# Kernel tuning notes

Hardware: AMD Instinct MI355X
Metric: run time of the kernel (lower is better)

Reference implementation:

```python
import jax, jax.numpy as jnp
import numpy as np
from jax import lax

EPS = 1e-20
BN_EPS = 1e-5
ATTN_SCALE = 2.8284271247461903  # sqrt(d_l=8)
NS = (32, 32, 32, 10)
DS = (8, 8, 8, 16)


def squash(x):
    # Efficient-CapsNet squash: (1 - 1/(exp(||x||)+eps)) * x/(||x||+eps)
    norm = jnp.linalg.norm(x, axis=-1, keepdims=True)
    return (1.0 - 1.0 / (jnp.exp(norm) + EPS)) * (x / (norm + EPS))


def conv2d(x, w, b, stride, groups=1):
    y = lax.conv_general_dilated(
        x, w, window_strides=(stride, stride), padding='VALID',
        dimension_numbers=('NCHW', 'OIHW', 'NCHW'),
        feature_group_count=groups)
    return y + b[None, :, None, None]


def bn(x, g, b, m, v):
    inv = g / jnp.sqrt(v + BN_EPS)
    return x * inv[None, :, None, None] + (b - m * inv)[None, :, None, None]


def fccaps(U_l, W):
    # U_l: (b, n_l, d_l), W: (n_l, n_h, d_l, d_h)
    U_hat = jnp.einsum('bij,ikjl->bikl', U_l, W)          # (b, n_l, n_h, d_h)
    A = jnp.einsum('bikl,bhkl->bhik', U_hat, U_hat)        # (b, n_l, n_l, n_h)
    A_sum = jnp.sum(A, axis=-2)                            # (b, n_l, n_h)
    C = jax.nn.softmax(A_sum / ATTN_SCALE, axis=-1)        # (b, n_l, n_h)
    U_h = jnp.einsum('bikl,bik->bkl', U_hat, C)            # (b, n_h, d_h)
    return squash(U_h)


def setup_inputs() -> dict:
    key = jax.random.key(0)
    ks = jax.random.split(key, 8)
    B = 512
    x = jax.random.normal(ks[0], (B, 1, 39, 39), dtype=jnp.float32)
    conv1_w = jax.random.normal(ks[1], (128, 1, 3, 3), jnp.float32) * 0.2
    conv1_b = jnp.zeros((128,), jnp.float32)
    conv2_w = jax.random.normal(ks[2], (256, 128, 3, 3), jnp.float32) * 0.04
    conv2_b = jnp.zeros((256,), jnp.float32)
    conv3_w = jax.random.normal(ks[3], (256, 1, 9, 9), jnp.float32) * 0.1  # depthwise
    conv3_b = jnp.zeros((256,), jnp.float32)
    bn1_g = jnp.ones((128,), jnp.float32); bn1_b = jnp.zeros((128,), jnp.float32)
    bn1_m = jnp.zeros((128,), jnp.float32); bn1_v = jnp.ones((128,), jnp.float32)
    bn2_g = jnp.ones((256,), jnp.float32); bn2_b = jnp.zeros((256,), jnp.float32)
    bn2_m = jnp.zeros((256,), jnp.float32); bn2_v = jnp.ones((256,), jnp.float32)
    # capsule weights, kaiming-ish scale sqrt(2/fan_in) with fan_in = n_h*d_l*d_h
    def caps_w(k, n_l, n_h, d_l, d_h):
        std = np.sqrt(2.0 / (n_h * d_l * d_h))
        return jax.random.normal(k, (n_l, n_h, d_l, d_h), jnp.float32) * std
    W1 = caps_w(ks[4], NS[0], NS[1], DS[0], DS[1])
    W2 = caps_w(ks[5], NS[1], NS[2], DS[1], DS[2])
    W3 = caps_w(ks[6], NS[2], NS[3], DS[2], DS[3])
    return dict(x=x, conv1_w=conv1_w, conv1_b=conv1_b,
                bn1_g=bn1_g, bn1_b=bn1_b, bn1_m=bn1_m, bn1_v=bn1_v,
                conv2_w=conv2_w, conv2_b=conv2_b,
                bn2_g=bn2_g, bn2_b=bn2_b, bn2_m=bn2_m, bn2_v=bn2_v,
                conv3_w=conv3_w, conv3_b=conv3_b, W1=W1, W2=W2, W3=W3)


def reference(x, conv1_w, conv1_b, bn1_g, bn1_b, bn1_m, bn1_v,
              conv2_w, conv2_b, bn2_g, bn2_b, bn2_m, bn2_v,
              conv3_w, conv3_b, W1, W2, W3):
    h = jax.nn.relu(bn(conv2d(x, conv1_w, conv1_b, 2), bn1_g, bn1_b, bn1_m, bn1_v))
    h = jax.nn.relu(bn(conv2d(h, conv2_w, conv2_b, 2), bn2_g, bn2_b, bn2_m, bn2_v))
    h = conv2d(h, conv3_w, conv3_b, 1, groups=256)        # (B, 256, 1, 1)
    u = h.reshape(h.shape[0], NS[0], DS[0])                # (B, 32, 8)
    u = squash(u)
    for W in (W1, W2, W3):
        u = fccaps(u, W)
    return u  # (B, 10, 16)
```

## Files before the change

kernel.cpp:

```cpp
#include <hip/hip_runtime.h>


typedef __attribute__((ext_vector_type(8))) short short8;
typedef __attribute__((ext_vector_type(4))) float f32x4;

__device__ __forceinline__ ushort f2bf(float x) {
    uint u = __float_as_uint(x);
    return (ushort)((u + 0x7FFFu + ((u >> 16) & 1u)) >> 16);
}
__device__ __forceinline__ void bfsplit(float x, ushort& h, ushort& l) {
    h = f2bf(x);
    float hf = __uint_as_float(((uint)h) << 16);
    l = f2bf(x - hf);
}

__global__ __launch_bounds__(256) void k_prep(
    const float* __restrict__ w2, uint* __restrict__ Bt,
    const float* __restrict__ w3, float* __restrict__ w3T,
    const float* __restrict__ W1, const float* __restrict__ W2,
    const float* __restrict__ W3, float* __restrict__ Wr1,
    float* __restrict__ Wr2, float* __restrict__ Wr3) {
    __shared__ __align__(16) float wbuf[64 * 288];
    const int b = blockIdx.x, t = threadIdx.x;
    if (b < 144) {
        const int sidx = b >> 2, coq = b & 3;
        const int chunk = sidx / 9, tap = sidx - chunk * 9;
        const int co0 = coq * 64;
        for (int idx = t; idx < 4608; idx += 256) {
            const int n = idx / 72, q = idx - n * 72;
            ((float4*)wbuf)[n * 72 + q] =
                *(const float4*)(w2 + (size_t)(co0 + n) * 1152 + chunk * 288 + q * 4);
        }
        __syncthreads();
        const int n = t & 63, dg = (t >> 6) * 4;
        const int cot = coq >> 1, nn = ((coq & 1) * 64) + n;
        uint* dst = Bt + (size_t)(sidx * 2 + cot) * 4096;
#pragma unroll
        for (int dd = 0; dd < 4; ++dd) {
            const int d = dg + dd;
            const float x = wbuf[n * 288 + (2 * d) * 9 + tap];
            const float y = wbuf[n * 288 + (2 * d + 1) * 9 + tap];
            ushort xh, xl, yh, yl;
            bfsplit(x, xh, xl);
            bfsplit(y, yl == yl ? yh : yh, yl);
            bfsplit(y, yh, yl);
            dst[nn * 16 + d]        = (uint)xh | ((uint)yh << 16);
            dst[2048 + nn * 16 + d] = (uint)xl | ((uint)yl << 16);
        }
    } else if (b < 225) {
        const int p = b - 144;
        w3T[p * 256 + t] = w3[t * 81 + p];
    } else {
        const int bb = b - 225;
        const int layer = bb >> 5, blk = bb & 31;
        const float* src = layer == 0 ? W1 : (layer == 1 ? W2 : W3);
        float* dst = layer == 0 ? Wr1 : (layer == 1 ? Wr2 : Wr3);
        const int d_h = (layer == 2) ? 16 : 8;
        const int total = (layer == 2) ? 5120 : 8192;
        for (int idx = blk * 256 + t; idx < 8 * total; idx += 32 * 256) {
            const int j = idx / total, e = idx - j * total;
            const int ik = e / d_h, l = e - ik * d_h;
            dst[idx] = src[(ik * 8 + j) * d_h + l];
        }
    }
}

__global__ __launch_bounds__(256) void k_conv1(
    const float* __restrict__ x, const float* __restrict__ w,
    const float* __restrict__ bias, const float* __restrict__ g,
    const float* __restrict__ bb, const float* __restrict__ bm,
    const float* __restrict__ bv, ushort* __restrict__ h1) {
    __shared__ __align__(16) float xs[1521];
    __shared__ float wls[1152];
    __shared__ float2 scsh[128];
    const int b = blockIdx.x, t = threadIdx.x;
    const float* xb = x + (size_t)b * 1521;
    for (int i = t; i < 1521; i += 256) xs[i] = xb[i];
    for (int i = t; i < 1152; i += 256) wls[i] = w[i];
    if (t < 128) {
        const float inv = g[t] * rsqrtf(bv[t] + 1e-5f);
        scsh[t] = make_float2(inv, bias[t] * inv + bb[t] - bm[t] * inv);
    }
    __syncthreads();
    const int o = t & 15, pg = t >> 4;
    float wr[8][9];
#pragma unroll
    for (int j = 0; j < 8; ++j)
#pragma unroll
        for (int k = 0; k < 9; ++k) wr[j][k] = wls[(o * 8 + j) * 9 + k];
    float2 ss[8];
#pragma unroll
    for (int j = 0; j < 8; ++j) ss[j] = scsh[o * 8 + j];
    const int chunk = o >> 2, ol = o & 3;
    ushort* cb = h1 + (size_t)b * 92416 + chunk * 23104;
    for (int p = pg; p < 361; p += 16) {
        const int y = p / 19, xq = p - y * 19;
        const int base = y * 78 + xq * 2;
        const float x0 = xs[base],      x1 = xs[base + 1],  x2 = xs[base + 2];
        const float x3 = xs[base + 39], x4 = xs[base + 40], x5 = xs[base + 41];
        const float x6 = xs[base + 78], x7 = xs[base + 79], x8 = xs[base + 80];
        short8 hs, ls;
#pragma unroll
        for (int j = 0; j < 8; ++j) {
            const float acc = x0 * wr[j][0] + x1 * wr[j][1] + x2 * wr[j][2] +
                              x3 * wr[j][3] + x4 * wr[j][4] + x5 * wr[j][5] +
                              x6 * wr[j][6] + x7 * wr[j][7] + x8 * wr[j][8];
            const float v = fmaxf(fmaf(acc, ss[j].x, ss[j].y), 0.0f);
            ushort hh, lw;
            bfsplit(v, hh, lw);
            hs[j] = (short)hh;
            ls[j] = (short)lw;
        }
        if ((xq & 1) == 0) {
            const int pos = y * 10 + (xq >> 1);
            *(short8*)(cb + ol * 1520 + pos * 8)         = hs;
            *(short8*)(cb + 11552 + ol * 1520 + pos * 8) = ls;
        } else {
            const int pos = y * 9 + (xq >> 1);
            *(short8*)(cb + 6080 + ol * 1368 + pos * 8)  = hs;
            *(short8*)(cb + 17632 + ol * 1368 + pos * 8) = ls;
        }
    }
}

__global__ __launch_bounds__(256, 3) void k_conv2(
    const uint* __restrict__ h1u, const uint* __restrict__ Bt,
    const float* __restrict__ g,
    const float* __restrict__ bb, const float* __restrict__ bm,
    const float* __restrict__ bv, const float* __restrict__ bias,
    const float* __restrict__ w3T, float* __restrict__ Uws) {
    __shared__ __align__(16) uint raw[11552];
    __shared__ float ured[128];
    const int t = threadIdx.x;
    const int lane = t & 63, wave = t >> 6;
    const int ln15 = lane & 15, lq = lane >> 4;
    const int wm = (wave >> 1) * 48, wn = (wave & 1) * 64;
    const int gg = blockIdx.x;
    const int bi  = ((gg >> 4) << 3) | (gg & 7);
    const int cot = (gg >> 3) & 1;
    const int co0 = cot * 128;

    int PE[3], PO[3];
#pragma unroll
    for (int i = 0; i < 3; ++i) {
        const int m = wm + i * 16 + ln15;
        const int p = m < 81 ? m : 80;
        const int oh = p / 9, ow = p - oh * 9;
        PE[i] = lq * 760 + oh * 80 + ow * 4;
        PO[i] = 3040 + lq * 684 + oh * 72 + ow * 4;
    }
    int BRDg[4];
#pragma unroll
    for (int j = 0; j < 4; ++j) {
        const int n = wn + j * 16 + ln15;
        BRDg[j] = n * 16 + lq * 4;
    }

    f32x4 acc[3][4] = {};
    uint4 Bn[8];
    {
        const uint* bp = Bt + (size_t)cot * 4096;
#pragma unroll
        for (int j = 0; j < 4; ++j) {
            Bn[j]     = *(const uint4*)(bp + BRDg[j]);
            Bn[4 + j] = *(const uint4*)(bp + 2048 + BRDg[j]);
        }
    }

#pragma unroll
    for (int c = 0; c < 4; ++c) {
        __syncthreads();
        {
            const uint4* src = (const uint4*)(h1u + (size_t)(bi * 4 + c) * 11552);
            uint4* dst = (uint4*)raw;
            uint4 tmp[11];
#pragma unroll
            for (int k = 0; k < 11; ++k) tmp[k] = src[t + k * 256];
            const bool extra = (t < 72);
            uint4 te;
            if (extra) te = src[t + 11 * 256];
#pragma unroll
            for (int k = 0; k < 11; ++k) dst[t + k * 256] = tmp[k];
            if (extra) dst[t + 11 * 256] = te;
        }
        __syncthreads();
        short8 a_h[3];
#pragma unroll
        for (int i = 0; i < 3; ++i)
            a_h[i] = *reinterpret_cast<const short8*>(raw + PE[i]);
#pragma unroll
        for (int tap = 0; tap < 9; ++tap) {
            const int s = c * 9 + tap;
            uint4 Bc[8];
#pragma unroll
            for (int q = 0; q < 8; ++q) Bc[q] = Bn[q];
            if (s < 35) {
                const uint* bp = Bt + (size_t)((s + 1) * 2 + cot) * 4096;
#pragma unroll
                for (int j = 0; j < 4; ++j) {
                    Bn[j]     = *(const uint4*)(bp + BRDg[j]);
                    Bn[4 + j] = *(const uint4*)(bp + 2048 + BRDg[j]);
                }
            }
            const int kh = tap / 3, kw = tap - kh * 3;
            const int odd = kw & 1;
            const int sE = kh * 40 + (kw >> 1) * 4;
            const int sO = kh * 36;
            short8 a_l[3];
#pragma unroll
            for (int i = 0; i < 3; ++i) {
                const int addr = odd ? (PO[i] + sO) : (PE[i] + sE);
                a_l[i] = *reinterpret_cast<const short8*>(raw + addr + 5776);
            }
            short8 a_hn[3];
            if (tap < 8) {
                const int tap2 = tap + 1;
                const int kh2 = tap2 / 3, kw2 = tap2 - kh2 * 3;
                const int odd2 = kw2 & 1;
                const int sE2 = kh2 * 40 + (kw2 >> 1) * 4;
                const int sO2 = kh2 * 36;
#pragma unroll
                for (int i = 0; i < 3; ++i) {
                    const int addr2 = odd2 ? (PO[i] + sO2) : (PE[i] + sE2);
                    a_hn[i] = *reinterpret_cast<const short8*>(raw + addr2);
                }
            }
            short8 bh[4], bl[4];
#pragma unroll
            for (int j = 0; j < 4; ++j) {
                bh[j] = __builtin_bit_cast(short8, Bc[j]);
                bl[j] = __builtin_bit_cast(short8, Bc[4 + j]);
            }
#pragma unroll
            for (int i = 0; i < 3; ++i)
#pragma unroll
                for (int j = 0; j < 4; ++j)
                    acc[i][j] = __builtin_amdgcn_mfma_f32_16x16x32_bf16(a_h[i], bh[j], acc[i][j], 0, 0, 0);
#pragma unroll
            for (int i = 0; i < 3; ++i)
#pragma unroll
                for (int j = 0; j < 4; ++j)
                    acc[i][j] = __builtin_amdgcn_mfma_f32_16x16x32_bf16(a_h[i], bl[j], acc[i][j], 0, 0, 0);
#pragma unroll
            for (int i = 0; i < 3; ++i)
#pragma unroll
                for (int j = 0; j < 4; ++j)
                    acc[i][j] = __builtin_amdgcn_mfma_f32_16x16x32_bf16(a_l[i], bh[j], acc[i][j], 0, 0, 0);
            if (tap < 8) {
#pragma unroll
                for (int i = 0; i < 3; ++i) a_h[i] = a_hn[i];
            }
        }
    }

    float scj[4], shj[4];
#pragma unroll
    for (int j = 0; j < 4; ++j) {
        const int co = co0 + wn + j * 16 + ln15;
        const float inv = g[co] * rsqrtf(bv[co] + 1e-5f);
        scj[j] = inv;
        shj[j] = bias[co] * inv + bb[co] - bm[co] * inv;
    }
    float usum[4] = {0.f, 0.f, 0.f, 0.f};
#pragma unroll
    for (int i = 0; i < 3; ++i)
#pragma unroll
        for (int r = 0; r < 4; ++r) {
            const int m = wm + i * 16 + lq * 4 + r;
            if (m < 81) {
                const float* wrow = w3T + m * 256 + co0;
#pragma unroll
                for (int j = 0; j < 4; ++j) {
                    const int col = wn + j * 16 + ln15;
                    const float v = fmaxf(fmaf(acc[i][j][r], scj[j], shj[j]), 0.0f);
                    usum[j] = fmaf(v, wrow[col], usum[j]);
                }
            }
        }
#pragma unroll
    for (int j = 0; j < 4; ++j) {
        usum[j] += __shfl_xor(usum[j], 16);
        usum[j] += __shfl_xor(usum[j], 32);
    }
    if (lq == 0 && wm == 0) {
#pragma unroll
        for (int j = 0; j < 4; ++j) ured[(wn >> 6) * 64 + j * 16 + ln15] = usum[j];
    }
    __syncthreads();
    if (lq == 0 && wm == 48) {
#pragma unroll
        for (int j = 0; j < 4; ++j) {
            const int col = wn + j * 16 + ln15;
            Uws[(size_t)bi * 256 + co0 + col] =
                usum[j] + ured[(wn >> 6) * 64 + j * 16 + ln15];
        }
    }
}

__device__ __forceinline__ void fccaps_block(
    const int n_l, const int n_h, const int d_h, const float* __restrict__ Wr,
    float* U, float* Uh, float* Sv, float* Av, float* Cv, float* coefs,
    float* outU, const int t) {
    const int nkd = n_h * d_h;
    const int total = n_l * nkd;
    __syncthreads();
    for (int e = t; e < total; e += 256) {
        const int i = e / nkd;
        const float* up = U + i * 8;
        float acc = 0.0f;
#pragma unroll
        for (int j = 0; j < 8; ++j) acc += up[j] * Wr[j * total + e];
        Uh[e] = acc;
    }
    __syncthreads();
    for (int e = t; e < nkd; e += 256) {
        float acc = 0.0f;
        for (int i = 0; i < n_l; ++i) acc += Uh[i * nkd + e];
        Sv[e] = acc;
    }
    __syncthreads();
    for (int e = t; e < n_l * n_h; e += 256) {
        const int h = e / n_h, k = e - h * n_h;
        float acc = 0.0f;
        for (int l = 0; l < d_h; ++l)
            acc += Uh[h * nkd + k * d_h + l] * Sv[k * d_h + l];
        Av[e] = acc;
    }
    __syncthreads();
    {
        const int h = t >> 3, sub = t & 7;
        const float invs = 1.0f / 2.8284271247461903f;
        float mx = -1e30f;
        for (int k = sub; k < n_h; k += 8) mx = fmaxf(mx, Av[h * n_h + k]);
        mx = fmaxf(mx, __shfl_xor(mx, 1));
        mx = fmaxf(mx, __shfl_xor(mx, 2));
        mx = fmaxf(mx, __shfl_xor(mx, 4));
        float sum = 0.0f;
        for (int k = sub; k < n_h; k += 8) {
            const float ev = expf((Av[h * n_h + k] - mx) * invs);
            Cv[h * n_h + k] = ev;
            sum += ev;
        }
        sum += __shfl_xor(sum, 1);
        sum += __shfl_xor(sum, 2);
        sum += __shfl_xor(sum, 4);
        const float r = 1.0f / sum;
        for (int k = sub; k < n_h; k += 8) Cv[h * n_h + k] *= r;
    }
    __syncthreads();
    for (int e = t; e < nkd; e += 256) {
        const int k = e / d_h;
        float acc = 0.0f;
        for (int i = 0; i < n_l; ++i) acc += Uh[i * nkd + e] * Cv[i * n_h + k];
        Sv[e] = acc;
    }
    __syncthreads();
    if (t < n_h) {
        float ssq = 0.0f;
        for (int l = 0; l < d_h; ++l) { const float uv = Sv[t * d_h + l]; ssq += uv * uv; }
        const float n = sqrtf(ssq);
        coefs[t] = (1.0f - 1.0f / (expf(n) + 1e-20f)) / (n + 1e-20f);
    }
    __syncthreads();
    for (int e = t; e < nkd; e += 256) outU[e] = Sv[e] * coefs[e / d_h];
}

__global__ __launch_bounds__(256) void k_caps(
    const float* __restrict__ Uws, const float* __restrict__ b3,
    const float* __restrict__ Wr1, const float* __restrict__ Wr2,
    const float* __restrict__ Wr3, float* __restrict__ out) {
    __shared__ float U[256];
    __shared__ float Uh[8192];
    __shared__ float Sv[256];
    __shared__ float Av[1024];
    __shared__ float Cv[1024];
    __shared__ float coefs[32];
    const int b = blockIdx.x, t = threadIdx.x;
    U[t] = Uws[(size_t)b * 256 + t] + b3[t];
    __syncthreads();
    if (t < 32) {
        float ssq = 0.0f;
        for (int j = 0; j < 8; ++j) { const float uv = U[t * 8 + j]; ssq += uv * uv; }
        const float n = sqrtf(ssq);
        coefs[t] = (1.0f - 1.0f / (expf(n) + 1e-20f)) / (n + 1e-20f);
    }
    __syncthreads();
    U[t] *= coefs[t >> 3];
    fccaps_block(32, 32,  8, Wr1, U, Uh, Sv, Av, Cv, coefs, U, t);
    fccaps_block(32, 32,  8, Wr2, U, Uh, Sv, Av, Cv, coefs, U, t);
    fccaps_block(32, 10, 16, Wr3, U, Uh, Sv, Av, Cv, coefs, out + (size_t)b * 160, t);
}

extern "C" void kernel_launch(void* const* d_in, const int* in_sizes, int n_in,
                              void* d_out, int out_size, void* d_ws, size_t ws_size,
                              hipStream_t stream) {
    const float* x    = (const float*)d_in[0];
    const float* c1w  = (const float*)d_in[1];
    const float* c1b  = (const float*)d_in[2];
    const float* bn1g = (const float*)d_in[3];
    const float* bn1b = (const float*)d_in[4];
    const float* bn1m = (const float*)d_in[5];
    const float* bn1v = (const float*)d_in[6];
    const float* c2w  = (const float*)d_in[7];
    const float* c2b  = (const float*)d_in[8];
    const float* bn2g = (const float*)d_in[9];
    const float* bn2b = (const float*)d_in[10];
    const float* bn2m = (const float*)d_in[11];
    const float* bn2v = (const float*)d_in[12];
    const float* c3w  = (const float*)d_in[13];
    const float* c3b  = (const float*)d_in[14];
    const float* W1   = (const float*)d_in[15];
    const float* W2   = (const float*)d_in[16];
    const float* W3   = (const float*)d_in[17];
    float* out = (float*)d_out;
    uint*  wsu = (uint*)d_ws;
    float* wsf = (float*)d_ws;

    ushort* h1  = (ushort*)wsu;
    float*  Uws = wsf + 23658496;
    uint*   Bt  = wsu + 23789568;
    float*  w3T = wsf + 24084480;
    float*  Wr1 = wsf + 24105216;
    float*  Wr2 = wsf + 24170752;
    float*  Wr3 = wsf + 24236288;

    k_prep<<<dim3(321), 256, 0, stream>>>(c2w, Bt, c3w, w3T, W1, W2, W3,
                                          Wr1, Wr2, Wr3);
    k_conv1<<<dim3(512), 256, 0, stream>>>(x, c1w, c1b, bn1g, bn1b, bn1m, bn1v, h1);
    k_conv2<<<dim3(1024), 256, 0, stream>>>((const uint*)h1, Bt, bn2g, bn2b, bn2m, bn2v,
                                            c2b, w3T, Uws);
    k_caps<<<dim3(512), 256, 0, stream>>>(Uws, c3b, Wr1, Wr2, Wr3, out);
}
```

Measured before the change: 226.8 us.

## Fuse conv1 into conv2 by recomputing conv1 tiles in shared memory

Removes the separate conv1 kernel and its large bf16 hi/lo intermediate buffer in global memory. Each conv2 block now loads its input image into LDS and computes the conv1 + BN + ReLU channel chunk directly into the LDS tile it used to copy from global. BN1 scale/shift precompute moves into an extra k_prep block. The cost is that conv1 is recomputed twice per image, once for each of the two output-channel halves, and conv2 blocks carry extra LDS and registers, which may reduce occupancy.

```diff
diff --git a/kernel.cpp b/kernel.cpp
--- a/kernel.cpp
+++ b/kernel.cpp
@@ -2,6 +2,7 @@
 
 
 typedef __attribute__((ext_vector_type(8))) short short8;
+typedef __attribute__((ext_vector_type(4))) short bf16x4;
 typedef __attribute__((ext_vector_type(4))) float f32x4;
 
 __device__ __forceinline__ ushort f2bf(float x) {
@@ -19,7 +20,10 @@
     const float* __restrict__ w3, float* __restrict__ w3T,
     const float* __restrict__ W1, const float* __restrict__ W2,
     const float* __restrict__ W3, float* __restrict__ Wr1,
-    float* __restrict__ Wr2, float* __restrict__ Wr3) {
+    float* __restrict__ Wr2, float* __restrict__ Wr3,
+    const float* __restrict__ c1b, const float* __restrict__ g1,
+    const float* __restrict__ b1, const float* __restrict__ m1,
+    const float* __restrict__ v1, float2* __restrict__ sc1) {
     __shared__ __align__(16) float wbuf[64 * 288];
     const int b = blockIdx.x, t = threadIdx.x;
     if (b < 144) {
@@ -42,7 +46,6 @@
             const float y = wbuf[n * 288 + (2 * d + 1) * 9 + tap];
             ushort xh, xl, yh, yl;
             bfsplit(x, xh, xl);
-            bfsplit(y, yl == yl ? yh : yh, yl);
             bfsplit(y, yh, yl);
             dst[nn * 16 + d]        = (uint)xh | ((uint)yh << 16);
             dst[2048 + nn * 16 + d] = (uint)xl | ((uint)yl << 16);
@@ -50,7 +53,7 @@
     } else if (b < 225) {
         const int p = b - 144;
         w3T[p * 256 + t] = w3[t * 81 + p];
-    } else {
+    } else if (b < 321) {
         const int bb = b - 225;
         const int layer = bb >> 5, blk = bb & 31;
         const float* src = layer == 0 ? W1 : (layer == 1 ? W2 : W3);
@@ -62,74 +65,23 @@
             const int ik = e / d_h, l = e - ik * d_h;
             dst[idx] = src[(ik * 8 + j) * d_h + l];
         }
-    }
-}
-
-__global__ __launch_bounds__(256) void k_conv1(
-    const float* __restrict__ x, const float* __restrict__ w,
-    const float* __restrict__ bias, const float* __restrict__ g,
-    const float* __restrict__ bb, const float* __restrict__ bm,
-    const float* __restrict__ bv, ushort* __restrict__ h1) {
-    __shared__ __align__(16) float xs[1521];
-    __shared__ float wls[1152];
-    __shared__ float2 scsh[128];
-    const int b = blockIdx.x, t = threadIdx.x;
-    const float* xb = x + (size_t)b * 1521;
-    for (int i = t; i < 1521; i += 256) xs[i] = xb[i];
-    for (int i = t; i < 1152; i += 256) wls[i] = w[i];
-    if (t < 128) {
-        const float inv = g[t] * rsqrtf(bv[t] + 1e-5f);
-        scsh[t] = make_float2(inv, bias[t] * inv + bb[t] - bm[t] * inv);
-    }
-    __syncthreads();
-    const int o = t & 15, pg = t >> 4;
-    float wr[8][9];
-#pragma unroll
-    for (int j = 0; j < 8; ++j)
-#pragma unroll
-        for (int k = 0; k < 9; ++k) wr[j][k] = wls[(o * 8 + j) * 9 + k];
-    float2 ss[8];
-#pragma unroll
-    for (int j = 0; j < 8; ++j) ss[j] = scsh[o * 8 + j];
-    const int chunk = o >> 2, ol = o & 3;
-    ushort* cb = h1 + (size_t)b * 92416 + chunk * 23104;
-    for (int p = pg; p < 361; p += 16) {
-        const int y = p / 19, xq = p - y * 19;
-        const int base = y * 78 + xq * 2;
-        const float x0 = xs[base],      x1 = xs[base + 1],  x2 = xs[base + 2];
-        const float x3 = xs[base + 39], x4 = xs[base + 40], x5 = xs[base + 41];
-        const float x6 = xs[base + 78], x7 = xs[base + 79], x8 = xs[base + 80];
-        short8 hs, ls;
-#pragma unroll
-        for (int j = 0; j < 8; ++j) {
-            const float acc = x0 * wr[j][0] + x1 * wr[j][1] + x2 * wr[j][2] +
-                              x3 * wr[j][3] + x4 * wr[j][4] + x5 * wr[j][5] +
-                              x6 * wr[j][6] + x7 * wr[j][7] + x8 * wr[j][8];
-            const float v = fmaxf(fmaf(acc, ss[j].x, ss[j].y), 0.0f);
-            ushort hh, lw;
-            bfsplit(v, hh, lw);
-            hs[j] = (short)hh;
-            ls[j] = (short)lw;
-        }
-        if ((xq & 1) == 0) {
-            const int pos = y * 10 + (xq >> 1);
-            *(short8*)(cb + ol * 1520 + pos * 8)         = hs;
-            *(short8*)(cb + 11552 + ol * 1520 + pos * 8) = ls;
-        } else {
-            const int pos = y * 9 + (xq >> 1);
-            *(short8*)(cb + 6080 + ol * 1368 + pos * 8)  = hs;
-            *(short8*)(cb + 17632 + ol * 1368 + pos * 8) = ls;
+    } else {
+        if (t < 128) {
+            const float inv = g1[t] * rsqrtf(v1[t] + 1e-5f);
+            sc1[t] = make_float2(inv, c1b[t] * inv + b1[t] - m1[t] * inv);
         }
     }
 }
 
 __global__ __launch_bounds__(256, 3) void k_conv2(
-    const uint* __restrict__ h1u, const uint* __restrict__ Bt,
+    const float* __restrict__ x, const float* __restrict__ w1,
+    const float2* __restrict__ sc1, const uint* __restrict__ Bt,
     const float* __restrict__ g,
     const float* __restrict__ bb, const float* __restrict__ bm,
     const float* __restrict__ bv, const float* __restrict__ bias,
     const float* __restrict__ w3T, float* __restrict__ Uws) {
     __shared__ __align__(16) uint raw[11552];
+    __shared__ __align__(16) float xs[1521];
     __shared__ float ured[128];
     const int t = threadIdx.x;
     const int lane = t & 63, wave = t >> 6;
@@ -140,6 +92,11 @@
     const int cot = (gg >> 3) & 1;
     const int co0 = cot * 128;
 
+    const float* xb = x + (size_t)bi * 1521;
+    for (int i = t; i < 1521; i += 256) xs[i] = xb[i];
+
+    const int hc = t & 7, o2 = hc >> 1, half = hc & 1, pg = t >> 3;
+
     int PE[3], PO[3];
 #pragma unroll
     for (int i = 0; i < 3; ++i) {
@@ -169,21 +126,57 @@
 
 #pragma unroll
     for (int c = 0; c < 4; ++c) {
+        const int o = c * 4 + o2;
+        float wr[36];
+        {
+            const float4* wp = reinterpret_cast<const float4*>(w1 + o * 72 + half * 36);
+#pragma unroll
+            for (int q = 0; q < 9; ++q) {
+                const float4 wv = wp[q];
+                wr[q * 4 + 0] = wv.x; wr[q * 4 + 1] = wv.y;
+                wr[q * 4 + 2] = wv.z; wr[q * 4 + 3] = wv.w;
+            }
+        }
+        float2 ssv[4];
+#pragma unroll
+        for (int jj = 0; jj < 4; ++jj) ssv[jj] = sc1[o * 8 + half * 4 + jj];
+
         __syncthreads();
+
         {
-            const uint4* src = (const uint4*)(h1u + (size_t)(bi * 4 + c) * 11552);
-            uint4* dst = (uint4*)raw;
-            uint4 tmp[11];
-#pragma unroll
-            for (int k = 0; k < 11; ++k) tmp[k] = src[t + k * 256];
-            const bool extra = (t < 72);
-            uint4 te;
-            if (extra) te = src[t + 11 * 256];
-#pragma unroll
-            for (int k = 0; k < 11; ++k) dst[t + k * 256] = tmp[k];
-            if (extra) dst[t + 11 * 256] = te;
+            ushort* rawu = (ushort*)raw;
+            for (int p = pg; p < 361; p += 32) {
+                const int y = p / 19, xq = p - y * 19;
+                const int base = y * 78 + xq * 2;
+                const float x0 = xs[base],      x1 = xs[base + 1],  x2 = xs[base + 2];
+                const float x3 = xs[base + 39], x4 = xs[base + 40], x5 = xs[base + 41];
+                const float x6 = xs[base + 78], x7 = xs[base + 79], x8 = xs[base + 80];
+                bf16x4 hs, ls;
+#pragma unroll
+                for (int jj = 0; jj < 4; ++jj) {
+                    const float a = x0 * wr[jj * 9 + 0] + x1 * wr[jj * 9 + 1] +
+                                    x2 * wr[jj * 9 + 2] + x3 * wr[jj * 9 + 3] +
+                                    x4 * wr[jj * 9 + 4] + x5 * wr[jj * 9 + 5] +
+                                    x6 * wr[jj * 9 + 6] + x7 * wr[jj * 9 + 7] +
+                                    x8 * wr[jj * 9 + 8];
+                    const float v = fmaxf(fmaf(a, ssv[jj].x, ssv[jj].y), 0.0f);
+                    ushort hh, lw;
+                    bfsplit(v, hh, lw);
+                    hs[jj] = (short)hh;
+                    ls[jj] = (short)lw;
+                }
+                int ad;
+                if ((xq & 1) == 0) {
+                    ad = o2 * 1520 + (y * 10 + (xq >> 1)) * 8 + half * 4;
+                } else {
+                    ad = 6080 + o2 * 1368 + (y * 9 + (xq >> 1)) * 8 + half * 4;
+                }
+                *(bf16x4*)(rawu + ad)         = hs;
+                *(bf16x4*)(rawu + 11552 + ad) = ls;
+            }
         }
         __syncthreads();
+
         short8 a_h[3];
 #pragma unroll
         for (int i = 0; i < 3; ++i)
@@ -416,18 +409,19 @@
     uint*  wsu = (uint*)d_ws;
     float* wsf = (float*)d_ws;
 
-    ushort* h1  = (ushort*)wsu;
-    float*  Uws = wsf + 23658496;
-    uint*   Bt  = wsu + 23789568;
-    float*  w3T = wsf + 24084480;
-    float*  Wr1 = wsf + 24105216;
-    float*  Wr2 = wsf + 24170752;
-    float*  Wr3 = wsf + 24236288;
-
-    k_prep<<<dim3(321), 256, 0, stream>>>(c2w, Bt, c3w, w3T, W1, W2, W3,
-                                          Wr1, Wr2, Wr3);
-    k_conv1<<<dim3(512), 256, 0, stream>>>(x, c1w, c1b, bn1g, bn1b, bn1m, bn1v, h1);
-    k_conv2<<<dim3(1024), 256, 0, stream>>>((const uint*)h1, Bt, bn2g, bn2b, bn2m, bn2v,
+    float*  Uws = wsf;
+    uint*   Bt  = wsu + 131072;
+    float*  w3T = wsf + 425984;
+    float*  Wr1 = wsf + 446720;
+    float*  Wr2 = wsf + 512256;
+    float*  Wr3 = wsf + 577792;
+    float2* sc1 = (float2*)(wsf + 618752);
+
+    k_prep<<<dim3(322), 256, 0, stream>>>(c2w, Bt, c3w, w3T, W1, W2, W3,
+                                          Wr1, Wr2, Wr3,
+                                          c1b, bn1g, bn1b, bn1m, bn1v, sc1);
+    k_conv2<<<dim3(1024), 256, 0, stream>>>(x, c1w, sc1, Bt,
+                                            bn2g, bn2b, bn2m, bn2v,
                                             c2b, w3T, Uws);
     k_caps<<<dim3(512), 256, 0, stream>>>(Uws, c3b, Wr1, Wr2, Wr3, out);
 }
```

New measurement: 219.5 us. -3.2%, faster.
